# Optimization experiments

Hardware: AMD Instinct MI355X
Metric: run time of the kernel (lower is better)

## Reference

```python
import jax, jax.numpy as jnp
import numpy as np

F_DIM, H, O = 128, 256, 256
NQ, EQ = 64, 512
ND, ED = 50000, 600000

PARAM_SHAPES = [
    ("qW1", (F_DIM, H)), ("qb1", (H,)), ("qW2", (H, H)), ("qb2", (H,)),
    ("qW3", (H, H)),     ("qb3", (H,)), ("qW4", (H, O)), ("qb4", (O,)),
    ("dW1", (F_DIM, H)), ("db1", (H,)), ("dW2", (H, H)), ("db2", (H,)),
    ("dW3", (H, H)),     ("db3", (H,)), ("dW4", (H, O)), ("db4", (O,)),
    ("lW1", (2 * O, O)), ("lb1", (O,)),
    ("lW2", (O, O // 2)), ("lb2", (O // 2,)),
    ("lW3", (O // 2, 8)), ("lb3", (8,)),
]

def setup_inputs() -> dict:
    key = jax.random.key(0)
    ks = jax.random.split(key, 4 + len(PARAM_SHAPES))
    inp = {
        "query_in_feat": jax.random.normal(ks[0], (NQ, F_DIM), jnp.float32),
        "data_in_feat": jax.random.normal(ks[1], (ND, F_DIM), jnp.float32),
        "query_edge_list": jax.random.randint(ks[2], (2, EQ), 0, NQ),
        "data_edge_list": jax.random.randint(ks[3], (2, ED), 0, ND),
    }
    for i, (name, shape) in enumerate(PARAM_SHAPES):
        fan_in = shape[0] if len(shape) == 2 else 1
        inp[name] = jax.random.normal(ks[4 + i], shape, jnp.float32) * (1.0 / np.sqrt(fan_in))
    return inp

def _mlp2(x, W1, b1, W2, b2):
    return jnp.maximum(x @ W1 + b1, 0.0) @ W2 + b2

def _gin_conv(x, src, dst, W1, b1, W2, b2):
    # GINConv (eps=0): MLP(x_i + sum_{j->i} x_j); gather x[src], scatter-add at dst
    agg = jax.ops.segment_sum(x[src], dst, num_segments=x.shape[0])
    return _mlp2(x + agg, W1, b1, W2, b2)

def _gin(x, edge_index, p):
    src, dst = edge_index[0], edge_index[1]
    h = jnp.maximum(_gin_conv(x, src, dst, *p[:4]), 0.0)  # ReLU between convs
    return _gin_conv(h, src, dst, *p[4:])

def reference(query_in_feat, data_in_feat, query_edge_list, data_edge_list,
              qW1, qb1, qW2, qb2, qW3, qb3, qW4, qb4,
              dW1, db1, dW2, db2, dW3, db3, dW4, db4,
              lW1, lb1, lW2, lb2, lW3, lb3):
    qx = _gin(query_in_feat, query_edge_list, (qW1, qb1, qW2, qb2, qW3, qb3, qW4, qb4))
    dx = _gin(data_in_feat, data_edge_list, (dW1, db1, dW2, db2, dW3, db3, dW4, db4))
    # global_add_pool with batch = zeros -> single-graph sum
    qp = jnp.sum(qx, axis=0, keepdims=True)  # [1, O]
    dp = jnp.sum(dx, axis=0, keepdims=True)  # [1, O]
    h = jnp.concatenate([qp, dp], axis=1)    # [1, 2*O]
    h = jnp.maximum(h @ lW1 + lb1, 0.0)
    h = jnp.maximum(h @ lW2 + lb2, 0.0)
    h = jnp.maximum(h @ lW3 + lb3, 0.0)
    return h.reshape(1, 8)
```

## Files before the change

### kernel.cpp

```cpp
#include <hip/hip_runtime.h>
#include <hip/hip_bf16.h>


#define NQ 64
#define EQ 512
#define ND 50000
#define ED 600000
#define FDIM 128
#define HDIM 256

typedef __attribute__((ext_vector_type(8))) short short8;
typedef __attribute__((ext_vector_type(4))) float f32x4;
typedef __attribute__((ext_vector_type(2))) float floatx2;
typedef __attribute__((ext_vector_type(4))) unsigned short us4;
typedef __attribute__((ext_vector_type(2))) unsigned short us2;

__device__ __forceinline__ unsigned short f2bf(float f) {
    union { float f; unsigned u; } v; v.f = f;
    unsigned r = v.u + 0x7FFF + ((v.u >> 16) & 1);
    return (unsigned short)(r >> 16);
}
__device__ __forceinline__ float bf2f(unsigned short u) {
    union { unsigned u; float f; } v; v.u = ((unsigned)u) << 16;
    return v.f;
}


__global__ void zero_init(float4* __restrict__ p, int n16) {
    const int i = blockIdx.x * 256 + threadIdx.x;
    if (i < n16) p[i] = float4{0.f, 0.f, 0.f, 0.f};
}


struct PackDesc {
    const float* W[8];
    unsigned short* Wp[8];
    int KT[8];
    int start[9];
};

__device__ __forceinline__ void pack_unit(const PackDesc& pd, int unit, int l) {
    int m = 0;
    while (m < 7 && unit >= pd.start[m + 1]) ++m;
    const int local = unit - pd.start[m];
    const int KT = pd.KT[m];
    const int kt = local % KT;
    const int ct = local / KT;
    const float* W = pd.W[m];
    unsigned short* Wp = pd.Wp[m];
    const int row = kt * 32 + (l >> 4) * 8;
    const int col = ct * 16 + (l & 15);
    short8 v;
#pragma unroll
    for (int j = 0; j < 8; ++j) v[j] = (short)f2bf(W[(size_t)(row + j) * 256 + col]);
    *(short8*)(Wp + (((size_t)(ct * KT + kt)) * 64 + l) * 8) = v;
}


__global__ void prepass(const float* __restrict__ xd, const float* __restrict__ xq,
                        unsigned char* __restrict__ x8, long long nd4, long long n4,
                        int cvt_b, PackDesc pd, int pack_units, int pack_b,
                        const int* __restrict__ d_dst, int* __restrict__ d_deg,
                        const int* __restrict__ q_dst, int* __restrict__ q_deg,
                        int d_eb) {
    const int b = blockIdx.x;
    const int tid = threadIdx.x;
    if (b < cvt_b) {
        long long i = (long long)b * 256 + tid;
        if (i >= n4) return;
        const float* src = (i < nd4) ? (xd + i * 4) : (xq + (i - nd4) * 4);
        float4 v = *(const float4*)src;
        int p = __builtin_amdgcn_cvt_pk_fp8_f32(v.x, v.y, 0, false);
        p = __builtin_amdgcn_cvt_pk_fp8_f32(v.z, v.w, p, true);
        *(unsigned*)(x8 + i * 4) = (unsigned)p;
    } else if (b < cvt_b + pack_b) {
        const int unit = (b - cvt_b) * 4 + (tid >> 6);
        if (unit < pack_units) pack_unit(pd, unit, tid & 63);
    } else {
        const int cb = b - cvt_b - pack_b;
        if (cb < d_eb) {
            int e = cb * 256 + tid;
            if (e < ED) atomicAdd(&d_deg[d_dst[e]], 1);
        } else {
            int e = (cb - d_eb) * 256 + tid;
            if (e < EQ) atomicAdd(&q_deg[q_dst[e]], 1);
        }
    }
}


__device__ __forceinline__ void scan1_body(const int* deg, int* rowptr, int* bsum,
                                           int n, int blk) {
    __shared__ int sh[256];
    const int t = threadIdx.x;
    const int i = blk * 256 + t;
    const int v = (i < n) ? deg[i] : 0;
    sh[t] = v;
    __syncthreads();
    for (int off = 1; off < 256; off <<= 1) {
        int x = (t >= off) ? sh[t - off] : 0;
        __syncthreads();
        sh[t] += x;
        __syncthreads();
    }
    if (i < n) rowptr[i] = sh[t] - v;
    if (t == 255) bsum[blk] = sh[255];
}

__global__ void scan_phase1_both(const int* __restrict__ d_deg, int* __restrict__ d_rowptr,
                                 int* __restrict__ d_bsum,
                                 const int* __restrict__ q_deg, int* __restrict__ q_rowptr,
                                 int* __restrict__ q_bsum, int dblocks) {
    int b = blockIdx.x;
    if (b < dblocks) scan1_body(d_deg, d_rowptr, d_bsum, ND, b);
    else             scan1_body(q_deg, q_rowptr, q_bsum, NQ, b - dblocks);
}

__device__ __forceinline__ void scan2_body(const int* bsum, int* boff, int* rowptr_n, int nb) {
    __shared__ int sh[256];
    const int t = threadIdx.x;
    const int v = (t < nb) ? bsum[t] : 0;
    sh[t] = v;
    __syncthreads();
    for (int off = 1; off < 256; off <<= 1) {
        int x = (t >= off) ? sh[t - off] : 0;
        __syncthreads();
        sh[t] += x;
        __syncthreads();
    }
    if (t < nb) boff[t] = sh[t] - v;
    if (t == 255) *rowptr_n = sh[255];
}

__global__ void scan_phase2_both(const int* __restrict__ d_bsum, int* __restrict__ d_boff,
                                 int* __restrict__ d_rowptr_n, int d_nb,
                                 const int* __restrict__ q_bsum, int* __restrict__ q_boff,
                                 int* __restrict__ q_rowptr_n, int q_nb) {
    if (blockIdx.x == 0) scan2_body(d_bsum, d_boff, d_rowptr_n, d_nb);
    else                 scan2_body(q_bsum, q_boff, q_rowptr_n, q_nb);
}

__global__ void scan_phase3_both(int* __restrict__ d_rowptr, const int* __restrict__ d_boff,
                                 int* __restrict__ d_cursor,
                                 int* __restrict__ q_rowptr, const int* __restrict__ q_boff,
                                 int* __restrict__ q_cursor, int dblocks) {
    int b = blockIdx.x;
    if (b < dblocks) {
        int i = b * 256 + threadIdx.x;
        if (i < ND) {
            int r = d_rowptr[i] + d_boff[b];
            d_rowptr[i] = r; d_cursor[i] = r;
        }
    } else {
        int i = (b - dblocks) * 256 + threadIdx.x;
        if (i < NQ) {
            int r = q_rowptr[i] + q_boff[b - dblocks];
            q_rowptr[i] = r; q_cursor[i] = r;
        }
    }
}

__global__ void fill_csr_both(const int* __restrict__ d_src, const int* __restrict__ d_dst,
                              int* __restrict__ d_cursor, int* __restrict__ d_csrsrc,
                              const int* __restrict__ q_src, const int* __restrict__ q_dst,
                              int* __restrict__ q_cursor, int* __restrict__ q_csrsrc,
                              int dblocks) {
    int b = blockIdx.x;
    if (b < dblocks) {
        int e = b * 256 + threadIdx.x;
        if (e < ED) {
            int p = atomicAdd(&d_cursor[d_dst[e]], 1);
            d_csrsrc[p] = d_src[e];
        }
    } else {
        int e = (b - dblocks) * 256 + threadIdx.x;
        if (e < EQ) {
            int p = atomicAdd(&q_cursor[q_dst[e]], 1);
            q_csrsrc[p] = q_src[e];
        }
    }
}


__global__ void gin_agg_f8_128_dual(const unsigned char* __restrict__ xd,
                                    const int* __restrict__ rpd, const int* __restrict__ csd,
                                    unsigned short* __restrict__ od,
                                    const unsigned char* __restrict__ xq,
                                    const int* __restrict__ rpq, const int* __restrict__ csq,
                                    unsigned short* __restrict__ oq, int ndpair) {
    const unsigned char* x; const int* rowptr; const int* csr; unsigned short* out; int nb;
    if ((int)blockIdx.x < ndpair) { x = xd; rowptr = rpd; csr = csd; out = od; nb = blockIdx.x; }
    else { x = xq; rowptr = rpq; csr = csq; out = oq; nb = blockIdx.x - ndpair; }

    const int t = threadIdx.x;
    const int node = nb * 2 + (t >> 5);
    const int c = t & 31;

    const int beg = rowptr[node];
    const int end = rowptr[node + 1];

    float a0, a1, a2, a3;
    {
        const unsigned w = *(const unsigned*)(x + (size_t)node * 128 + c * 4);
        floatx2 lo = __builtin_amdgcn_cvt_pk_f32_fp8((int)w, false);
        floatx2 hi = __builtin_amdgcn_cvt_pk_f32_fp8((int)w, true);
        a0 = lo[0]; a1 = lo[1]; a2 = hi[0]; a3 = hi[1];
    }
    for (int j = beg; j < end; ++j) {
        const unsigned w = *(const unsigned*)(x + (size_t)csr[j] * 128 + c * 4);
        floatx2 lo = __builtin_amdgcn_cvt_pk_f32_fp8((int)w, false);
        floatx2 hi = __builtin_amdgcn_cvt_pk_f32_fp8((int)w, true);
        a0 += lo[0]; a1 += lo[1]; a2 += hi[0]; a3 += hi[1];
    }
    us4 r;
    r[0] = f2bf(a0); r[1] = f2bf(a1); r[2] = f2bf(a2); r[3] = f2bf(a3);
    *(us4*)(out + (size_t)node * 128 + c * 4) = r;
}


__global__ void gin_agg_f8_256_dual(const unsigned char* __restrict__ xd,
                                    const int* __restrict__ rpd, const int* __restrict__ csd,
                                    unsigned short* __restrict__ od,
                                    const unsigned char* __restrict__ xq,
                                    const int* __restrict__ rpq, const int* __restrict__ csq,
                                    unsigned short* __restrict__ oq) {
    const unsigned char* x; const int* rowptr; const int* csr; unsigned short* out; int node;
    if ((int)blockIdx.x < ND) { x = xd; rowptr = rpd; csr = csd; out = od; node = blockIdx.x; }
    else { x = xq; rowptr = rpq; csr = csq; out = oq; node = blockIdx.x - ND; }

    const int t = threadIdx.x;
    const int beg = rowptr[node];
    const int end = rowptr[node + 1];

    float a0, a1, a2, a3;
    {
        const unsigned w = *(const unsigned*)(x + (size_t)node * 256 + t * 4);
        floatx2 lo = __builtin_amdgcn_cvt_pk_f32_fp8((int)w, false);
        floatx2 hi = __builtin_amdgcn_cvt_pk_f32_fp8((int)w, true);
        a0 = lo[0]; a1 = lo[1]; a2 = hi[0]; a3 = hi[1];
    }
    int j = beg;
    for (; j + 1 < end; j += 2) {
        const unsigned w0 = *(const unsigned*)(x + (size_t)csr[j] * 256 + t * 4);
        const unsigned w1 = *(const unsigned*)(x + (size_t)csr[j + 1] * 256 + t * 4);
        floatx2 l0 = __builtin_amdgcn_cvt_pk_f32_fp8((int)w0, false);
        floatx2 h0 = __builtin_amdgcn_cvt_pk_f32_fp8((int)w0, true);
        floatx2 l1 = __builtin_amdgcn_cvt_pk_f32_fp8((int)w1, false);
        floatx2 h1 = __builtin_amdgcn_cvt_pk_f32_fp8((int)w1, true);
        a0 += l0[0] + l1[0]; a1 += l0[1] + l1[1];
        a2 += h0[0] + h1[0]; a3 += h0[1] + h1[1];
    }
    if (j < end) {
        const unsigned w0 = *(const unsigned*)(x + (size_t)csr[j] * 256 + t * 4);
        floatx2 l0 = __builtin_amdgcn_cvt_pk_f32_fp8((int)w0, false);
        floatx2 h0 = __builtin_amdgcn_cvt_pk_f32_fp8((int)w0, true);
        a0 += l0[0]; a1 += l0[1]; a2 += h0[0]; a3 += h0[1];
    }
    us4 r;
    r[0] = f2bf(a0); r[1] = f2bf(a1); r[2] = f2bf(a2); r[3] = f2bf(a3);
    *(us4*)(out + (size_t)node * 256 + t * 4) = r;
}


template <int KIN>
__global__ __launch_bounds__(256) void mlp_dual(
    const unsigned short* __restrict__ Ad,
    const unsigned short* __restrict__ W1pd, const float* __restrict__ b1d,
    const unsigned short* __restrict__ W2pd, const float* __restrict__ b2d,
    unsigned char* __restrict__ C8d, int ndb,
    const unsigned short* __restrict__ Aq,
    const unsigned short* __restrict__ W1pq, const float* __restrict__ b1q,
    const unsigned short* __restrict__ W2pq, const float* __restrict__ b2q,
    unsigned char* __restrict__ C8q) {
    constexpr int KT1 = KIN / 32;
    __shared__ __align__(16) unsigned short lds[64 * 256];

    const unsigned short* A; const unsigned short* W1p; const float* b1;
    const unsigned short* W2p; const float* b2;
    unsigned char* C8; int row0, N;
    if ((int)blockIdx.x < ndb) {
        A = Ad; W1p = W1pd; b1 = b1d; W2p = W2pd; b2 = b2d;
        C8 = C8d; row0 = blockIdx.x * 64; N = ND;
    } else {
        A = Aq; W1p = W1pq; b1 = b1q; W2p = W2pq; b2 = b2q;
        C8 = C8q; row0 = 0; N = NQ;
    }

    const int tid = threadIdx.x;
    const int lane = tid & 63;
    const int wv = tid >> 6;
    const int lrow = lane & 15;
    const int lk2 = (lane >> 4) * 8;
    const int nrows = (N - row0 < 64) ? (N - row0) : 64;

    for (int idx = tid; idx < nrows * (KIN / 8); idx += 256) {
        const int r = idx / (KIN / 8);
        const int k8 = (idx % (KIN / 8)) * 8;
        short8 v = *(const short8*)(A + (size_t)(row0 + r) * KIN + k8);
        unsigned byte = (unsigned)((r * KIN + k8) * 2) ^ (unsigned)((r & 7) << 4);
        *(short8*)((char*)lds + byte) = v;
    }
    __syncthreads();

    f32x4 acc1[4][4];
#pragma unroll
    for (int fm = 0; fm < 4; ++fm)
#pragma unroll
        for (int fn = 0; fn < 4; ++fn) acc1[fm][fn] = (f32x4)(0.f);

    const unsigned short* W1Base = W1p + ((size_t)(wv * 4) * KT1 * 64 + lane) * 8;
    for (int kt = 0; kt < KT1; ++kt) {
        short8 a[4], bf[4];
#pragma unroll
        for (int fm = 0; fm < 4; ++fm) {
            const int r = fm * 16 + lrow;
            unsigned byte = (unsigned)((r * KIN + kt * 32 + lk2) * 2) ^ (unsigned)((r & 7) << 4);
            a[fm] = *(const short8*)((const char*)lds + byte);
        }
#pragma unroll
        for (int fn = 0; fn < 4; ++fn)
            bf[fn] = *(const short8*)(W1Base + ((size_t)fn * KT1 + kt) * 64 * 8);
#pragma unroll
        for (int fm = 0; fm < 4; ++fm)
#pragma unroll
            for (int fn = 0; fn < 4; ++fn)
                acc1[fm][fn] = __builtin_amdgcn_mfma_f32_16x16x32_bf16(
                    a[fm], bf[fn], acc1[fm][fn], 0, 0, 0);
    }
    __syncthreads();

#pragma unroll
    for (int fn = 0; fn < 4; ++fn) {
        const int col = wv * 64 + fn * 16 + lrow;
        const float bv = b1[col];
#pragma unroll
        for (int fm = 0; fm < 4; ++fm) {
            const int rbase = fm * 16 + (lane >> 4) * 4;
#pragma unroll
            for (int r = 0; r < 4; ++r) {
                const int row = rbase + r;
                const float v = fmaxf(acc1[fm][fn][r] + bv, 0.f);
                unsigned byte = (unsigned)((row * 256 + col) * 2) ^ (unsigned)((row & 7) << 4);
                *(unsigned short*)((char*)lds + byte) = f2bf(v);
            }
        }
    }
    __syncthreads();

    f32x4 acc2[4][4];
#pragma unroll
    for (int fm = 0; fm < 4; ++fm)
#pragma unroll
        for (int fn = 0; fn < 4; ++fn) acc2[fm][fn] = (f32x4)(0.f);

    const unsigned short* W2Base = W2p + ((size_t)(wv * 4) * 8 * 64 + lane) * 8;
    for (int kt = 0; kt < 8; ++kt) {
        short8 a[4], bf[4];
#pragma unroll
        for (int fm = 0; fm < 4; ++fm) {
            const int r = fm * 16 + lrow;
            unsigned byte = (unsigned)((r * 256 + kt * 32 + lk2) * 2) ^ (unsigned)((r & 7) << 4);
            a[fm] = *(const short8*)((const char*)lds + byte);
        }
#pragma unroll
        for (int fn = 0; fn < 4; ++fn)
            bf[fn] = *(const short8*)(W2Base + ((size_t)fn * 8 + kt) * 64 * 8);
#pragma unroll
        for (int fm = 0; fm < 4; ++fm)
#pragma unroll
            for (int fn = 0; fn < 4; ++fn)
                acc2[fm][fn] = __builtin_amdgcn_mfma_f32_16x16x32_bf16(
                    a[fm], bf[fn], acc2[fm][fn], 0, 0, 0);
    }

#pragma unroll
    for (int fn = 0; fn < 4; ++fn) {
        const int col = wv * 64 + fn * 16 + lrow;
        const float bv = b2[col];
#pragma unroll
        for (int fm = 0; fm < 4; ++fm) {
            const int rbase = row0 + fm * 16 + (lane >> 4) * 4;
#pragma unroll
            for (int r = 0; r < 4; ++r) {
                const int row = rbase + r;
                if (row < N) {
                    float v = fmaxf(acc2[fm][fn][r] + bv, 0.f);
                    unsigned p = (unsigned)__builtin_amdgcn_cvt_pk_fp8_f32(v, v, 0, false);
                    C8[(size_t)row * 256 + col] = (unsigned char)(p & 0xff);
                }
            }
        }
    }
}


__global__ __launch_bounds__(256) void t1pool_dual(
    const unsigned short* __restrict__ Ad,
    const unsigned short* __restrict__ W1pd, const float* __restrict__ b1d,
    float* __restrict__ poold, int ndb,
    const unsigned short* __restrict__ Aq,
    const unsigned short* __restrict__ W1pq, const float* __restrict__ b1q,
    float* __restrict__ poolq) {
    const unsigned short* A; const unsigned short* W1p; const float* b1;
    float* pool; int row0, N;
    if ((int)blockIdx.x < ndb) {
        A = Ad; W1p = W1pd; b1 = b1d; pool = poold; row0 = blockIdx.x * 64; N = ND;
    } else {
        A = Aq; W1p = W1pq; b1 = b1q; pool = poolq; row0 = 0; N = NQ;
    }

    const int tid = threadIdx.x;
    const int lane = tid & 63;
    const int wv = tid >> 6;
    const int lrow = lane & 15;
    const int lk2 = (lane >> 4) * 8;

    f32x4 acc[4][4];
#pragma unroll
    for (int fm = 0; fm < 4; ++fm)
#pragma unroll
        for (int fn = 0; fn < 4; ++fn) acc[fm][fn] = (f32x4)(0.f);

    const unsigned short* W1Base = W1p + ((size_t)(wv * 4) * 8 * 64 + lane) * 8;
    const unsigned short* Alane = A + (size_t)(row0 + lrow) * 256 + lk2;

#pragma unroll
    for (int kt = 0; kt < 8; ++kt) {
        short8 a[4], bf[4];
#pragma unroll
        for (int fm = 0; fm < 4; ++fm)
            a[fm] = *(const short8*)(Alane + (size_t)(fm * 16) * 256 + kt * 32);
#pragma unroll
        for (int fn = 0; fn < 4; ++fn)
            bf[fn] = *(const short8*)(W1Base + ((size_t)fn * 8 + kt) * 64 * 8);
#pragma unroll
        for (int fm = 0; fm < 4; ++fm)
#pragma unroll
            for (int fn = 0; fn < 4; ++fn)
                acc[fm][fn] = __builtin_amdgcn_mfma_f32_16x16x32_bf16(
                    a[fm], bf[fn], acc[fm][fn], 0, 0, 0);
    }

#pragma unroll
    for (int fn = 0; fn < 4; ++fn) {
        const int col = wv * 64 + fn * 16 + lrow;
        const float bv = b1[col];
        float ps = 0.f;
#pragma unroll
        for (int fm = 0; fm < 4; ++fm) {
            const int rbase = row0 + fm * 16 + (lane >> 4) * 4;
#pragma unroll
            for (int r = 0; r < 4; ++r) {
                const int row = rbase + r;
                if (row < N) ps += fmaxf(acc[fm][fn][r] + bv, 0.f);
            }
        }
        ps += __shfl_xor(ps, 16);
        ps += __shfl_xor(ps, 32);
        if ((lane >> 4) == 0) atomicAdd(&pool[col], ps);
    }
}


__global__ void head_w4(const float* __restrict__ poolT1,
                        const float* __restrict__ qW4, const float* __restrict__ qb4,
                        const float* __restrict__ dW4, const float* __restrict__ db4,
                        float* __restrict__ s0) {
    const int b = blockIdx.x;
    const int m = b >> 3;
    const int ks = (b & 7) * 32;
    const int t = threadIdx.x;
    const float* W = m ? dW4 : qW4;
    const float* P = poolT1 + (m ? 256 : 0);
    float acc = 0.f;
    for (int k = ks; k < ks + 32; ++k) acc += P[k] * W[(size_t)k * 256 + t];
    if ((b & 7) == 0) acc += m ? (float)ND * db4[t] : (float)NQ * qb4[t];
    atomicAdd(&s0[m * 256 + t], acc);
}

__global__ void head_l1(const float* __restrict__ s0, const float* __restrict__ lW1,
                        const float* __restrict__ lb1, float* __restrict__ s1) {
    const int ks = blockIdx.x * 32;
    const int t = threadIdx.x;
    float acc = 0.f;
    for (int k = ks; k < ks + 32; ++k) acc += s0[k] * lW1[(size_t)k * 256 + t];
    if (blockIdx.x == 0) acc += lb1[t];
    atomicAdd(&s1[t], acc);
}

__global__ void head_l2(const float* __restrict__ s1, const float* __restrict__ lW2,
                        const float* __restrict__ lb2, float* __restrict__ s2) {
    const int ks = blockIdx.x * 32;
    const int t = threadIdx.x;
    float acc = 0.f;
    for (int k = ks; k < ks + 32; ++k) acc += fmaxf(s1[k], 0.f) * lW2[(size_t)k * 128 + t];
    if (blockIdx.x == 0) acc += lb2[t];
    atomicAdd(&s2[t], acc);
}

__global__ void head_l3(const float* __restrict__ s2, const float* __restrict__ lW3,
                        const float* __restrict__ lb3, float* __restrict__ out) {
    const int t = threadIdx.x;
    if (t < 8) {
        float acc = lb3[t];
        for (int k = 0; k < 128; ++k) acc += fmaxf(s2[k], 0.f) * lW3[k * 8 + t];
        out[t] = fmaxf(acc, 0.f);
    }
}


extern "C" void kernel_launch(void* const* d_in, const int* in_sizes, int n_in,
                              void* d_out, int out_size, void* d_ws, size_t ws_size,
                              hipStream_t stream) {
    const float* q_x  = (const float*)d_in[0];
    const float* d_x  = (const float*)d_in[1];
    const int*   q_el = (const int*)d_in[2];
    const int*   d_el = (const int*)d_in[3];
    const float* qW1 = (const float*)d_in[4];  const float* qb1 = (const float*)d_in[5];
    const float* qW2 = (const float*)d_in[6];  const float* qb2 = (const float*)d_in[7];
    const float* qW3 = (const float*)d_in[8];  const float* qb3 = (const float*)d_in[9];
    const float* qW4 = (const float*)d_in[10]; const float* qb4 = (const float*)d_in[11];
    const float* dW1 = (const float*)d_in[12]; const float* db1 = (const float*)d_in[13];
    const float* dW2 = (const float*)d_in[14]; const float* db2 = (const float*)d_in[15];
    const float* dW3 = (const float*)d_in[16]; const float* db3 = (const float*)d_in[17];
    const float* dW4 = (const float*)d_in[18]; const float* db4 = (const float*)d_in[19];
    const float* lW1 = (const float*)d_in[20]; const float* lb1 = (const float*)d_in[21];
    const float* lW2 = (const float*)d_in[22]; const float* lb2 = (const float*)d_in[23];
    const float* lW3 = (const float*)d_in[24]; const float* lb3 = (const float*)d_in[25];
    (void)in_sizes; (void)n_in; (void)out_size; (void)ws_size;

    const int* q_src = q_el;  const int* q_dst = q_el + EQ;
    const int* d_src = d_el;  const int* d_dst = d_el + ED;

    char* wsb = (char*)d_ws;
    size_t off = 0;
    auto alloc = [&](size_t bytes) { void* p = wsb + off; off += (bytes + 255) & ~(size_t)255; return p; };

    unsigned char*  x8d = (unsigned char*)alloc((size_t)ND * FDIM);
    unsigned char*  x8q = (unsigned char*)alloc((size_t)NQ * FDIM);
    unsigned short* dag = (unsigned short*)alloc((size_t)ND * FDIM * 2);
    unsigned short* qag = (unsigned short*)alloc((size_t)NQ * FDIM * 2);
    unsigned char*  h8d = (unsigned char*)alloc((size_t)ND * HDIM);
    unsigned char*  h8q = (unsigned char*)alloc((size_t)NQ * HDIM);
    unsigned short* had = (unsigned short*)alloc((size_t)ND * HDIM * 2);
    unsigned short* haq = (unsigned short*)alloc((size_t)(NQ + 64) * HDIM * 2);
    float* poolT1 = (float*)alloc(512 * 4);
    float* s0     = (float*)alloc(512 * 4);
    float* s1     = (float*)alloc(256 * 4);
    float* s2     = (float*)alloc(128 * 4);
    int* d_deg    = (int*)alloc((size_t)ND * 4);
    int* q_deg    = (int*)alloc((size_t)NQ * 4);
    char* zero_end = wsb + off;
    int* d_rowptr = (int*)alloc((size_t)(ND + 1) * 4);
    int* d_cursor = (int*)alloc((size_t)ND * 4);
    int* d_csrsrc = (int*)alloc((size_t)ED * 4);
    int* d_bsum   = (int*)alloc(256 * 4);
    int* d_boff   = (int*)alloc(256 * 4);
    int* q_rowptr = (int*)alloc((size_t)(NQ + 1) * 4);
    int* q_cursor = (int*)alloc((size_t)NQ * 4);
    int* q_csrsrc = (int*)alloc((size_t)EQ * 4);
    int* q_bsum   = (int*)alloc(256 * 4);
    int* q_boff   = (int*)alloc(256 * 4);
    unsigned short* pdW1 = (unsigned short*)alloc((size_t)FDIM * 256 * 2);
    unsigned short* pdW2 = (unsigned short*)alloc((size_t)HDIM * 256 * 2);
    unsigned short* pdW3 = (unsigned short*)alloc((size_t)HDIM * 256 * 2);
    unsigned short* pqW1 = (unsigned short*)alloc((size_t)FDIM * 256 * 2);
    unsigned short* pqW2 = (unsigned short*)alloc((size_t)HDIM * 256 * 2);
    unsigned short* pqW3 = (unsigned short*)alloc((size_t)HDIM * 256 * 2);

    {
        const size_t zb = (size_t)(zero_end - (char*)poolT1);
        const int n16 = (int)(zb / 16);
        zero_init<<<(n16 + 255) / 256, 256, 0, stream>>>((float4*)poolT1, n16);
    }

    const int d_eb = (ED + 255) / 256;
    const int q_eb = (EQ + 255) / 256;
    const int d_nb = (ND + 255) / 256;
    const int q_nb = (NQ + 255) / 256;
    {
        PackDesc pd;
        const float* Ws[6] = {dW1, dW2, dW3, qW1, qW2, qW3};
        unsigned short* Wps[6] = {pdW1, pdW2, pdW3, pqW1, pqW2, pqW3};
        int kts[6] = {4, 8, 8, 4, 8, 8};
        int s = 0;
        for (int i = 0; i < 6; ++i) {
            pd.W[i] = Ws[i]; pd.Wp[i] = Wps[i]; pd.KT[i] = kts[i];
            pd.start[i] = s; s += 16 * kts[i];
        }
        for (int i = 6; i < 8; ++i) { pd.W[i] = dW1; pd.Wp[i] = pdW1; pd.KT[i] = 4; pd.start[i] = s; }
        pd.start[8] = s;
        const int pack_units = s;
        const int pack_b = (s + 3) / 4;
        long long nd4 = (long long)ND * FDIM / 4;
        long long n4 = nd4 + (long long)NQ * FDIM / 4;
        const int cvt_b = (int)((n4 + 255) / 256);
        prepass<<<cvt_b + pack_b + d_eb + q_eb, 256, 0, stream>>>(
            d_x, q_x, x8d, nd4, n4, cvt_b, pd, pack_units, pack_b,
            d_dst, d_deg, q_dst, q_deg, d_eb);
    }

    scan_phase1_both<<<d_nb + q_nb, 256, 0, stream>>>(d_deg, d_rowptr, d_bsum,
                                                      q_deg, q_rowptr, q_bsum, d_nb);
    scan_phase2_both<<<2, 256, 0, stream>>>(d_bsum, d_boff, d_rowptr + ND, d_nb,
                                            q_bsum, q_boff, q_rowptr + NQ, q_nb);
    scan_phase3_both<<<d_nb + q_nb, 256, 0, stream>>>(d_rowptr, d_boff, d_cursor,
                                                      q_rowptr, q_boff, q_cursor, d_nb);
    fill_csr_both<<<d_eb + q_eb, 256, 0, stream>>>(d_src, d_dst, d_cursor, d_csrsrc,
                                                   q_src, q_dst, q_cursor, q_csrsrc, d_eb);

    const int ndpair = ND / 2;
    const int qpair = NQ / 2;
    const int ndb = (ND + 63) / 64;

    gin_agg_f8_128_dual<<<ndpair + qpair, 64, 0, stream>>>(
        x8d, d_rowptr, d_csrsrc, dag, x8q, q_rowptr, q_csrsrc, qag, ndpair);
    mlp_dual<FDIM><<<ndb + 1, 256, 0, stream>>>(
        dag, pdW1, db1, pdW2, db2, h8d, ndb,
        qag, pqW1, qb1, pqW2, qb2, h8q);

    gin_agg_f8_256_dual<<<ND + NQ, 64, 0, stream>>>(
        h8d, d_rowptr, d_csrsrc, had, h8q, q_rowptr, q_csrsrc, haq);
    t1pool_dual<<<ndb + 1, 256, 0, stream>>>(
        had, pdW3, db3, poolT1 + 256, ndb,
        haq, pqW3, qb3, poolT1);

    head_w4<<<16, 256, 0, stream>>>(poolT1, qW4, qb4, dW4, db4, s0);
    head_l1<<<16, 256, 0, stream>>>(s0, lW1, lb1, s1);
    head_l2<<<8, 128, 0, stream>>>(s1, lW2, lb2, s2);
    head_l3<<<1, 64, 0, stream>>>(s2, lW3, lb3, (float*)d_out);
}
```

Measured before the change: 228.5 us.

## Split MLP kernels across eight waves and fuse final head layers

The two MFMA MLP kernels now launch 512 threads per block. Each of the eight waves owns 32 output columns instead of 64, which halves the per-wave accumulator registers and doubles the waves available to hide latency. The last two head layers are merged into one single-block kernel that keeps the intermediate in shared memory, removing one launch and the atomic intermediate buffer. The larger blocks may lower how many blocks fit per CU, and each wave now reads the A tile for only half as many columns, so A-fragment reuse per LDS or global load drops.

New measurement: 231.3 us. Within noise of the previous version (+1.2%).

```diff
diff --git a/kernel.cpp b/kernel.cpp
--- a/kernel.cpp
+++ b/kernel.cpp
@@ -263,7 +263,7 @@
 
 
 template <int KIN>
-__global__ __launch_bounds__(256) void mlp_dual(
+__global__ __launch_bounds__(512) void mlp_dual(
     const unsigned short* __restrict__ Ad,
     const unsigned short* __restrict__ W1pd, const float* __restrict__ b1d,
     const unsigned short* __restrict__ W2pd, const float* __restrict__ b2d,
@@ -293,7 +293,7 @@
     const int lk2 = (lane >> 4) * 8;
     const int nrows = (N - row0 < 64) ? (N - row0) : 64;
 
-    for (int idx = tid; idx < nrows * (KIN / 8); idx += 256) {
+    for (int idx = tid; idx < nrows * (KIN / 8); idx += 512) {
         const int r = idx / (KIN / 8);
         const int k8 = (idx % (KIN / 8)) * 8;
         short8 v = *(const short8*)(A + (size_t)(row0 + r) * KIN + k8);
@@ -302,15 +302,15 @@
     }
     __syncthreads();
 
-    f32x4 acc1[4][4];
+    f32x4 acc1[4][2];
 #pragma unroll
     for (int fm = 0; fm < 4; ++fm)
 #pragma unroll
-        for (int fn = 0; fn < 4; ++fn) acc1[fm][fn] = (f32x4)(0.f);
-
-    const unsigned short* W1Base = W1p + ((size_t)(wv * 4) * KT1 * 64 + lane) * 8;
+        for (int fn = 0; fn < 2; ++fn) acc1[fm][fn] = (f32x4)(0.f);
+
+    const unsigned short* W1Base = W1p + ((size_t)(wv * 2) * KT1 * 64 + lane) * 8;
     for (int kt = 0; kt < KT1; ++kt) {
-        short8 a[4], bf[4];
+        short8 a[4], bf[2];
 #pragma unroll
         for (int fm = 0; fm < 4; ++fm) {
             const int r = fm * 16 + lrow;
@@ -318,20 +318,20 @@
             a[fm] = *(const short8*)((const char*)lds + byte);
         }
 #pragma unroll
-        for (int fn = 0; fn < 4; ++fn)
+        for (int fn = 0; fn < 2; ++fn)
             bf[fn] = *(const short8*)(W1Base + ((size_t)fn * KT1 + kt) * 64 * 8);
 #pragma unroll
         for (int fm = 0; fm < 4; ++fm)
 #pragma unroll
-            for (int fn = 0; fn < 4; ++fn)
+            for (int fn = 0; fn < 2; ++fn)
                 acc1[fm][fn] = __builtin_amdgcn_mfma_f32_16x16x32_bf16(
                     a[fm], bf[fn], acc1[fm][fn], 0, 0, 0);
     }
     __syncthreads();
 
 #pragma unroll
-    for (int fn = 0; fn < 4; ++fn) {
-        const int col = wv * 64 + fn * 16 + lrow;
+    for (int fn = 0; fn < 2; ++fn) {
+        const int col = wv * 32 + fn * 16 + lrow;
         const float bv = b1[col];
 #pragma unroll
         for (int fm = 0; fm < 4; ++fm) {
@@ -347,15 +347,15 @@
     }
     __syncthreads();
 
-    f32x4 acc2[4][4];
+    f32x4 acc2[4][2];
 #pragma unroll
     for (int fm = 0; fm < 4; ++fm)
 #pragma unroll
-        for (int fn = 0; fn < 4; ++fn) acc2[fm][fn] = (f32x4)(0.f);
-
-    const unsigned short* W2Base = W2p + ((size_t)(wv * 4) * 8 * 64 + lane) * 8;
+        for (int fn = 0; fn < 2; ++fn) acc2[fm][fn] = (f32x4)(0.f);
+
+    const unsigned short* W2Base = W2p + ((size_t)(wv * 2) * 8 * 64 + lane) * 8;
     for (int kt = 0; kt < 8; ++kt) {
-        short8 a[4], bf[4];
+        short8 a[4], bf[2];
 #pragma unroll
         for (int fm = 0; fm < 4; ++fm) {
             const int r = fm * 16 + lrow;
@@ -363,19 +363,19 @@
             a[fm] = *(const short8*)((const char*)lds + byte);
         }
 #pragma unroll
-        for (int fn = 0; fn < 4; ++fn)
+        for (int fn = 0; fn < 2; ++fn)
             bf[fn] = *(const short8*)(W2Base + ((size_t)fn * 8 + kt) * 64 * 8);
 #pragma unroll
         for (int fm = 0; fm < 4; ++fm)
 #pragma unroll
-            for (int fn = 0; fn < 4; ++fn)
+            for (int fn = 0; fn < 2; ++fn)
                 acc2[fm][fn] = __builtin_amdgcn_mfma_f32_16x16x32_bf16(
                     a[fm], bf[fn], acc2[fm][fn], 0, 0, 0);
     }
 
 #pragma unroll
-    for (int fn = 0; fn < 4; ++fn) {
-        const int col = wv * 64 + fn * 16 + lrow;
+    for (int fn = 0; fn < 2; ++fn) {
+        const int col = wv * 32 + fn * 16 + lrow;
         const float bv = b2[col];
 #pragma unroll
         for (int fm = 0; fm < 4; ++fm) {
@@ -394,7 +394,7 @@
 }
 
 
-__global__ __launch_bounds__(256) void t1pool_dual(
+__global__ __launch_bounds__(512) void t1pool_dual(
     const unsigned short* __restrict__ Ad,
     const unsigned short* __restrict__ W1pd, const float* __restrict__ b1d,
     float* __restrict__ poold, int ndb,
@@ -415,35 +415,35 @@
     const int lrow = lane & 15;
     const int lk2 = (lane >> 4) * 8;
 
-    f32x4 acc[4][4];
+    f32x4 acc[4][2];
 #pragma unroll
     for (int fm = 0; fm < 4; ++fm)
 #pragma unroll
-        for (int fn = 0; fn < 4; ++fn) acc[fm][fn] = (f32x4)(0.f);
-
-    const unsigned short* W1Base = W1p + ((size_t)(wv * 4) * 8 * 64 + lane) * 8;
+        for (int fn = 0; fn < 2; ++fn) acc[fm][fn] = (f32x4)(0.f);
+
+    const unsigned short* W1Base = W1p + ((size_t)(wv * 2) * 8 * 64 + lane) * 8;
     const unsigned short* Alane = A + (size_t)(row0 + lrow) * 256 + lk2;
 
 #pragma unroll
     for (int kt = 0; kt < 8; ++kt) {
-        short8 a[4], bf[4];
+        short8 a[4], bf[2];
 #pragma unroll
         for (int fm = 0; fm < 4; ++fm)
             a[fm] = *(const short8*)(Alane + (size_t)(fm * 16) * 256 + kt * 32);
 #pragma unroll
-        for (int fn = 0; fn < 4; ++fn)
+        for (int fn = 0; fn < 2; ++fn)
             bf[fn] = *(const short8*)(W1Base + ((size_t)fn * 8 + kt) * 64 * 8);
 #pragma unroll
         for (int fm = 0; fm < 4; ++fm)
 #pragma unroll
-            for (int fn = 0; fn < 4; ++fn)
+            for (int fn = 0; fn < 2; ++fn)
                 acc[fm][fn] = __builtin_amdgcn_mfma_f32_16x16x32_bf16(
                     a[fm], bf[fn], acc[fm][fn], 0, 0, 0);
     }
 
 #pragma unroll
-    for (int fn = 0; fn < 4; ++fn) {
-        const int col = wv * 64 + fn * 16 + lrow;
+    for (int fn = 0; fn < 2; ++fn) {
+        const int col = wv * 32 + fn * 16 + lrow;
         const float bv = b1[col];
         float ps = 0.f;
 #pragma unroll
@@ -488,23 +488,20 @@
     atomicAdd(&s1[t], acc);
 }
 
-__global__ void head_l2(const float* __restrict__ s1, const float* __restrict__ lW2,
-                        const float* __restrict__ lb2, float* __restrict__ s2) {
-    const int ks = blockIdx.x * 32;
+__global__ void head_l23(const float* __restrict__ s1,
+                         const float* __restrict__ lW2, const float* __restrict__ lb2,
+                         const float* __restrict__ lW3, const float* __restrict__ lb3,
+                         float* __restrict__ out) {
+    __shared__ float sh2[128];
     const int t = threadIdx.x;
-    float acc = 0.f;
-    for (int k = ks; k < ks + 32; ++k) acc += fmaxf(s1[k], 0.f) * lW2[(size_t)k * 128 + t];
-    if (blockIdx.x == 0) acc += lb2[t];
-    atomicAdd(&s2[t], acc);
-}
-
-__global__ void head_l3(const float* __restrict__ s2, const float* __restrict__ lW3,
-                        const float* __restrict__ lb3, float* __restrict__ out) {
-    const int t = threadIdx.x;
+    float acc = lb2[t];
+    for (int k = 0; k < 256; ++k) acc += fmaxf(s1[k], 0.f) * lW2[(size_t)k * 128 + t];
+    sh2[t] = fmaxf(acc, 0.f);
+    __syncthreads();
     if (t < 8) {
-        float acc = lb3[t];
-        for (int k = 0; k < 128; ++k) acc += fmaxf(s2[k], 0.f) * lW3[k * 8 + t];
-        out[t] = fmaxf(acc, 0.f);
+        float a = lb3[t];
+        for (int k = 0; k < 128; ++k) a += sh2[k] * lW3[k * 8 + t];
+        out[t] = fmaxf(a, 0.f);
     }
 }
 
@@ -547,7 +544,6 @@
     float* poolT1 = (float*)alloc(512 * 4);
     float* s0     = (float*)alloc(512 * 4);
     float* s1     = (float*)alloc(256 * 4);
-    float* s2     = (float*)alloc(128 * 4);
     int* d_deg    = (int*)alloc((size_t)ND * 4);
     int* q_deg    = (int*)alloc((size_t)NQ * 4);
     char* zero_end = wsb + off;
@@ -615,18 +611,17 @@
 
     gin_agg_f8_128_dual<<<ndpair + qpair, 64, 0, stream>>>(
         x8d, d_rowptr, d_csrsrc, dag, x8q, q_rowptr, q_csrsrc, qag, ndpair);
-    mlp_dual<FDIM><<<ndb + 1, 256, 0, stream>>>(
+    mlp_dual<FDIM><<<ndb + 1, 512, 0, stream>>>(
         dag, pdW1, db1, pdW2, db2, h8d, ndb,
         qag, pqW1, qb1, pqW2, qb2, h8q);
 
     gin_agg_f8_256_dual<<<ND + NQ, 64, 0, stream>>>(
         h8d, d_rowptr, d_csrsrc, had, h8q, q_rowptr, q_csrsrc, haq);
-    t1pool_dual<<<ndb + 1, 256, 0, stream>>>(
+    t1pool_dual<<<ndb + 1, 512, 0, stream>>>(
         had, pdW3, db3, poolT1 + 256, ndb,
         haq, pqW3, qb3, poolT1);
 
     head_w4<<<16, 256, 0, stream>>>(poolT1, qW4, qb4, dW4, db4, s0);
     head_l1<<<16, 256, 0, stream>>>(s0, lW1, lb1, s1);
-    head_l2<<<8, 128, 0, stream>>>(s1, lW2, lb2, s2);
-    head_l3<<<1, 64, 0, stream>>>(s2, lW3, lb3, (float*)d_out);
-}
+    head_l23<<<1, 128, 0, stream>>>(s1, lW2, lb2, lW3, lb3, (float*)d_out);
+}
```
